# Kernel tuning notes

Hardware: AMD Instinct MI355X
Metric: run time of the kernel (lower is better)

The kernel has to match this reference:

```python
import jax, jax.numpy as jnp
import numpy as np


def _positional_embedding(C, M, dtype):
    # pe[pos, 0::2] = sin(pos*div), pe[pos, 1::2] = cos(pos*div)
    pos = jnp.arange(M, dtype=jnp.float32)[:, None]                      # [M,1]
    div = jnp.exp(jnp.arange(0, C, 2, dtype=jnp.float32) * (-np.log(10000.0) / C))  # [C/2]
    ang = pos * div                                                      # [M,C/2]
    pe = jnp.stack([jnp.sin(ang), jnp.cos(ang)], axis=-1).reshape(M, C)  # interleave
    return pe.T.astype(dtype)                                            # [C,M]


def setup_inputs() -> dict:
    key = jax.random.key(0)
    k1, k2, k3 = jax.random.split(key, 3)
    B, C, M, K = 64, 512, 1024, 5
    h_in = jax.random.normal(k1, (B, C, 1, M), dtype=jnp.float32)
    conv_w = jax.random.normal(k2, (C, K), dtype=jnp.float32) * 0.1
    conv_b = jax.random.normal(k3, (C,), dtype=jnp.float32) * 0.1
    return {"h_in": h_in, "conv_w": conv_w, "conv_b": conv_b}


def reference(h_in, conv_w, conv_b):
    B, C, _, M = h_in.shape
    K = conv_w.shape[1]
    p = (K - 1) // 2
    dt = h_in.dtype

    hb = h_in                                              # pre-PE copy
    pe = _positional_embedding(C, M, dt)                   # [C,M]
    x = h_in + pe[None, :, None, :]                        # [B,C,1,M]

    # adaptive avg pool to 1 over (H,W)
    y = jnp.mean(x, axis=(2, 3))                           # [B,C]
    # unfold along channel axis with padding p, window K
    y_pad = jnp.pad(y, ((0, 0), (p, p)))                   # [B,C+2p]
    idx = jnp.arange(C)[:, None] + jnp.arange(K)[None, :]  # [C,K]
    y_unf = y_pad[:, idx]                                  # [B,C,K]
    # grouped conv1d -> per-channel dot over window, then sigmoid gate
    gate = jax.nn.sigmoid(jnp.einsum('bck,ck->bc', y_unf, conv_w) + conv_b)  # [B,C]

    h = x * gate[:, :, None, None]                         # dropout = identity (eval)

    hs = h[:, :, 0, :]                                     # [B,C,M]
    hbs = hb[:, :, 0, :]                                   # [B,C,M]
    I_hat = (jnp.eye(M, dtype=dt) / M) - (1.0 / (M * M))   # [M,M] centering matrix

    t1 = jnp.einsum('bcm,mn->bcn', hs, I_hat)
    t2 = jnp.einsum('bcm,mn->bcn', hbs, I_hat)
    cov = (jnp.einsum('bcn,bdn->bcd', t1, hs)
           + jnp.einsum('bcn,bdn->bcd', t2, hbs)
           + jnp.eye(C, dtype=dt) * 1e-8)                  # [B,C,C]
    return cov
```

## Files before the change

kernel.cpp:

```cpp
#include <hip/hip_runtime.h>
#include <hip/hip_bf16.h>
#include <math.h>

#define B_N 64
#define C_N 512
#define M_N 1024

typedef __attribute__((ext_vector_type(8))) short bf16x8;
typedef __attribute__((ext_vector_type(4))) float f32x4;
typedef __attribute__((ext_vector_type(16))) float f32x16;

__device__ __forceinline__ float b2f(unsigned short u) {
  unsigned int x = ((unsigned int)u) << 16;
  return __builtin_bit_cast(float, x);
}
__device__ __forceinline__ unsigned short f2b(float f) {
  unsigned int x = __builtin_bit_cast(unsigned int, f);
  unsigned int lsb = (x >> 16) & 1u;
  x += 0x7fffu + lsb;
  return (unsigned short)(x >> 16);
}
__device__ __forceinline__ float bround(float f) { return b2f(f2b(f)); }

typedef __attribute__((address_space(1))) const unsigned int gas_uint;
typedef __attribute__((address_space(3))) unsigned int las_uint;
__device__ __forceinline__ void async_ld(const void* g, const void* l) {
  __builtin_amdgcn_global_load_lds((gas_uint*)(uintptr_t)g,
                                   (las_uint*)(unsigned int)(uintptr_t)l, 16, 0, 0);
}

__global__ void k_detect(const unsigned short* __restrict__ p, int* __restrict__ flag) {
  unsigned short u = p[threadIdx.x];
  int e = (u >> 7) & 0xff;
  int pl = (u == 0) || (e >= 110 && e <= 134);
  int cnt = __syncthreads_count(pl);
  if (threadIdx.x == 0) *flag = (cnt >= 208) ? 1 : 0;
}

__global__ void k_mode(const int* __restrict__ flag, int wsOK, int* __restrict__ mode) {
  if (threadIdx.x == 0) *mode = (*flag == 1 && wsOK) ? 1 : 0;
}

__global__ void k_pe(unsigned short* __restrict__ pe) {
  int idx = blockIdx.x * 256 + threadIdx.x;
  int c = idx >> 10, m = idx & 1023;
  float freq = expf((float)(c & ~1) * (-9.210340371976184f / 512.0f));
  float ang = (float)m * freq;
  float v = (c & 1) ? cosf(ang) : sinf(ang);
  pe[idx] = f2b(v);
}

__global__ void k_pesum(const unsigned short* __restrict__ pe, float* __restrict__ pesum) {
  int lane = threadIdx.x & 63;
  int row = blockIdx.x * 4 + (threadIdx.x >> 6);
  float s = 0.f;
  const uint4* p = (const uint4*)(pe + (size_t)row * M_N);
  for (int j = 0; j < 2; j++) {
    union { uint4 v; unsigned short u[8]; } a; a.v = p[j * 64 + lane];
    for (int k = 0; k < 8; k++) s += b2f(a.u[k]);
  }
  for (int off = 32; off; off >>= 1) s += __shfl_down(s, off);
  if (lane == 0) pesum[row] = s;
}

__global__ void k_sums(const void* __restrict__ hin, const int* __restrict__ flag,
                       const float* __restrict__ pesum, float* __restrict__ rx,
                       float* __restrict__ rb) {
  int lane = threadIdx.x & 63;
  int row = blockIdx.x * 4 + (threadIdx.x >> 6);
  int f = *flag;
  float s = 0.f;
  if (f) {
    const uint4* h = (const uint4*)((const unsigned short*)hin + (size_t)row * M_N);
    for (int j = 0; j < 2; j++) {
      union { uint4 v; unsigned short u[8]; } a; a.v = h[j * 64 + lane];
      for (int k = 0; k < 8; k++) s += b2f(a.u[k]);
    }
  } else {
    const float4* h = (const float4*)((const float*)hin + (size_t)row * M_N);
    for (int j = 0; j < 4; j++) {
      float4 v = h[j * 64 + lane];
      s += v.x + v.y + v.z + v.w;
    }
  }
  for (int off = 32; off; off >>= 1) s += __shfl_down(s, off);
  if (lane == 0) { rb[row] = s; rx[row] = s + pesum[row & (C_N - 1)]; }
}

__global__ void k_gate(const void* __restrict__ wp, const void* __restrict__ bp,
                       const int* __restrict__ flag, const float* __restrict__ rx,
                       float* __restrict__ gate) {
  int idx = blockIdx.x * 256 + threadIdx.x;
  int b = idx >> 9, c = idx & (C_N - 1);
  int f = *flag;
  float acc = 0.f;
  for (int k = 0; k < 5; ++k) {
    int cc = c + k - 2;
    if (cc < 0 || cc >= C_N) continue;
    float y = rx[b * C_N + cc] * (1.0f / 1024.0f);
    float w;
    if (f) { y = bround(y); w = b2f(((const unsigned short*)wp)[c * 5 + k]); }
    else   { w = ((const float*)wp)[c * 5 + k]; }
    acc += y * w;
  }
  float bias = f ? b2f(((const unsigned short*)bp)[c]) : ((const float*)bp)[c];
  float s = f ? bround(bround(acc) + bias) : (acc + bias);
  float g = 1.0f / (1.0f + expf(-s));
  if (f) g = bround(g);
  gate[idx] = g;
}

__global__ void k_prep(const void* __restrict__ hin, const unsigned short* __restrict__ pe,
                       const int* __restrict__ mode, unsigned short* __restrict__ X) {
  if (*mode != 1) return;
  size_t e = ((size_t)blockIdx.x * 256 + threadIdx.x) * 8;
  int cm = (int)(e & ((size_t)C_N * M_N - 1));
  union { uint4 v; unsigned short u[8]; } a, p, r;
  a.v = *(const uint4*)((const unsigned short*)hin + e);
  p.v = *(const uint4*)(pe + cm);
  for (int k = 0; k < 8; k++) r.u[k] = f2b(b2f(a.u[k]) + b2f(p.u[k]));
  *(uint4*)(X + e) = r.v;
}

__global__ __launch_bounds__(256, 2)
void k_cov2(const unsigned short* __restrict__ X, const void* __restrict__ hin,
            const int* __restrict__ mode, const float* __restrict__ rx,
            const float* __restrict__ rb, const float* __restrict__ gate,
            void* __restrict__ out) {
  if (*mode != 1) return;
  __shared__ unsigned short tiles[4][128 * 32];

  const unsigned short* H = (const unsigned short*)hin;
  int t = threadIdx.x;
  int lane = t & 63, w = t >> 6;
  int b = blockIdx.z;
  int cblk = blockIdx.y * 128, dblk = blockIdx.x * 128;

  const unsigned short* src = (w & 1) ? H : X;
  int rowbase = (w & 2) ? dblk : cblk;
  int gcol = (lane & 3) ^ ((lane >> 3) & 3);
  const unsigned short* gp = src + (size_t)b * (C_N * M_N)
                           + (size_t)(rowbase + (lane >> 2)) * M_N + gcol * 8;

  int wr = (w >> 1) * 64, wc = (w & 1) * 64;
  int fr = lane & 31, L5 = lane >> 5;
  int sw = (fr >> 1) & 3;

  f32x16 a1[2][2], a2[2][2];
  for (int i = 0; i < 2; i++)
    for (int j = 0; j < 2; j++)
      for (int r = 0; r < 16; r++) { a1[i][j][r] = 0.f; a2[i][j][r] = 0.f; }

  for (int kk = 0; kk < M_N; kk += 32) {
    const unsigned short* g0 = gp + kk;
    for (int g = 0; g < 8; g++)
      async_ld(g0 + (size_t)g * (16 * M_N), &tiles[w][g * 512]);
    __syncthreads();

    for (int ks = 0; ks < 2; ks++) {
      int kc = (ks * 2 + L5);
      bf16x8 aX[2], aH[2], bX[2], bH[2];
      for (int i = 0; i < 2; i++) {
        int R = wr + i * 32 + fr;
        int off = R * 32 + (kc ^ sw) * 8;
        aX[i] = *(const bf16x8*)&tiles[0][off];
        aH[i] = *(const bf16x8*)&tiles[1][off];
      }
      for (int j = 0; j < 2; j++) {
        int D = wc + j * 32 + fr;
        int off = D * 32 + (kc ^ sw) * 8;
        bX[j] = *(const bf16x8*)&tiles[2][off];
        bH[j] = *(const bf16x8*)&tiles[3][off];
      }
      for (int i = 0; i < 2; i++)
        for (int j = 0; j < 2; j++) {
          a1[i][j] = __builtin_amdgcn_mfma_f32_32x32x16_bf16(aX[i], bX[j], a1[i][j], 0, 0, 0);
          a2[i][j] = __builtin_amdgcn_mfma_f32_32x32x16_bf16(aH[i], bH[j], a2[i][j], 0, 0, 0);
        }
    }
    __syncthreads();
  }

  const float invM = 1.0f / 1024.0f, invM2 = invM * invM;
  const float* gb = gate + b * C_N;
  const float* rxb = rx + b * C_N;
  const float* rbb = rb + b * C_N;
  unsigned short* o16 = (unsigned short*)out;
  for (int i = 0; i < 2; i++)
    for (int j = 0; j < 2; j++) {
      int d = dblk + wc + j * 32 + (lane & 31);
      float gd = gb[d], rxd = rxb[d], rbd = rbb[d];
      for (int reg = 0; reg < 16; reg++) {
        int row = (reg & 3) + 8 * (reg >> 2) + 4 * L5;
        int c = cblk + wr + i * 32 + row;
        float v = gb[c] * gd * (a1[i][j][reg] * invM - rxb[c] * rxd * invM2)
                + (a2[i][j][reg] * invM - rbb[c] * rbd * invM2);
        if (c == d) v += 1e-8f;
        o16[((size_t)b * C_N + c) * C_N + d] = f2b(v);
      }
    }
}

__global__ __launch_bounds__(256, 2)
void k_cov(const void* __restrict__ hin, const unsigned short* __restrict__ pe,
           const int* __restrict__ flag, const int* __restrict__ mode,
           const float* __restrict__ rx, const float* __restrict__ rb,
           const float* __restrict__ gate, void* __restrict__ out) {
  if (*mode != 0) return;
  __shared__ unsigned short sXa[128 * 40];
  __shared__ unsigned short sHa[128 * 40];
  __shared__ unsigned short sXb[128 * 40];
  __shared__ unsigned short sHb[128 * 40];

  int t = threadIdx.x;
  int b = blockIdx.z;
  int cblk = blockIdx.y * 128, dblk = blockIdx.x * 128;
  int f = *flag;
  int lane = t & 63, wave = t >> 6;
  int wr = (wave >> 1) * 64, wc = (wave & 1) * 64;
  int fr = lane & 15, fk = (lane >> 4) * 8;
  int sr = t >> 1, sc = (t & 1) * 16;

  f32x4 acc1[4][4], acc2[4][4];
  const f32x4 z = {0.f, 0.f, 0.f, 0.f};
  for (int i = 0; i < 4; i++)
    for (int j = 0; j < 4; j++) { acc1[i][j] = z; acc2[i][j] = z; }

  const size_t hb0 = (size_t)b * C_N * M_N;
  const unsigned short* peA = pe + (size_t)(cblk + sr) * M_N + sc;
  const unsigned short* peB = pe + (size_t)(dblk + sr) * M_N + sc;
  const unsigned short* hA16 = (const unsigned short*)hin + hb0 + (size_t)(cblk + sr) * M_N + sc;
  const unsigned short* hB16 = (const unsigned short*)hin + hb0 + (size_t)(dblk + sr) * M_N + sc;
  const float* hA32 = (const float*)hin + hb0 + (size_t)(cblk + sr) * M_N + sc;
  const float* hB32 = (const float*)hin + hb0 + (size_t)(dblk + sr) * M_N + sc;

  union U { uint4 v[2]; unsigned short u[16]; };

  for (int kk = 0; kk < M_N; kk += 32) {
    U pa, pb, wxa, wha, wxb, whb;
    {
      const uint4* ppa = reinterpret_cast<const uint4*>(peA + kk);
      pa.v[0] = ppa[0]; pa.v[1] = ppa[1];
      const uint4* ppb = reinterpret_cast<const uint4*>(peB + kk);
      pb.v[0] = ppb[0]; pb.v[1] = ppb[1];
    }
    if (f) {
      U ua, ub;
      const uint4* qa = reinterpret_cast<const uint4*>(hA16 + kk);
      ua.v[0] = qa[0]; ua.v[1] = qa[1];
      const uint4* qb = reinterpret_cast<const uint4*>(hB16 + kk);
      ub.v[0] = qb[0]; ub.v[1] = qb[1];
      for (int e = 0; e < 16; e++) {
        wha.u[e] = ua.u[e];
        whb.u[e] = ub.u[e];
        wxa.u[e] = f2b(b2f(ua.u[e]) + b2f(pa.u[e]));
        wxb.u[e] = f2b(b2f(ub.u[e]) + b2f(pb.u[e]));
      }
    } else {
      float fa[16], fb[16];
      const float4* qa = reinterpret_cast<const float4*>(hA32 + kk);
      const float4* qb = reinterpret_cast<const float4*>(hB32 + kk);
      for (int e = 0; e < 4; e++) {
        float4 va = qa[e], vb = qb[e];
        fa[4 * e + 0] = va.x; fa[4 * e + 1] = va.y; fa[4 * e + 2] = va.z; fa[4 * e + 3] = va.w;
        fb[4 * e + 0] = vb.x; fb[4 * e + 1] = vb.y; fb[4 * e + 2] = vb.z; fb[4 * e + 3] = vb.w;
      }
      for (int e = 0; e < 16; e++) {
        wha.u[e] = f2b(fa[e]);
        whb.u[e] = f2b(fb[e]);
        wxa.u[e] = f2b(fa[e] + b2f(pa.u[e]));
        wxb.u[e] = f2b(fb[e] + b2f(pb.u[e]));
      }
    }
    {
      uint4* d0 = reinterpret_cast<uint4*>(&sXa[sr * 40 + sc]);
      d0[0] = wxa.v[0]; d0[1] = wxa.v[1];
      uint4* d1 = reinterpret_cast<uint4*>(&sHa[sr * 40 + sc]);
      d1[0] = wha.v[0]; d1[1] = wha.v[1];
      uint4* d2 = reinterpret_cast<uint4*>(&sXb[sr * 40 + sc]);
      d2[0] = wxb.v[0]; d2[1] = wxb.v[1];
      uint4* d3 = reinterpret_cast<uint4*>(&sHb[sr * 40 + sc]);
      d3[0] = whb.v[0]; d3[1] = whb.v[1];
    }
    __syncthreads();

    bf16x8 bX[4], bH[4];
    for (int j = 0; j < 4; j++) {
      int dr = wc + j * 16 + fr;
      bX[j] = *reinterpret_cast<const bf16x8*>(&sXb[dr * 40 + fk]);
      bH[j] = *reinterpret_cast<const bf16x8*>(&sHb[dr * 40 + fk]);
    }
    for (int i = 0; i < 4; i++) {
      int cr = wr + i * 16 + fr;
      bf16x8 aX = *reinterpret_cast<const bf16x8*>(&sXa[cr * 40 + fk]);
      bf16x8 aH = *reinterpret_cast<const bf16x8*>(&sHa[cr * 40 + fk]);
      for (int j = 0; j < 4; j++) {
        acc1[i][j] = __builtin_amdgcn_mfma_f32_16x16x32_bf16(aX, bX[j], acc1[i][j], 0, 0, 0);
        acc2[i][j] = __builtin_amdgcn_mfma_f32_16x16x32_bf16(aH, bH[j], acc2[i][j], 0, 0, 0);
      }
    }
    __syncthreads();
  }

  const float invM = 1.0f / 1024.0f;
  const float invM2 = invM * invM;
  const float* gb = gate + b * C_N;
  const float* rxb = rx + b * C_N;
  const float* rbb = rb + b * C_N;
  for (int i = 0; i < 4; i++) {
    for (int r = 0; r < 4; r++) {
      int c = cblk + wr + i * 16 + (lane >> 4) * 4 + r;
      float gc = gb[c], rxc = rxb[c], rbc = rbb[c];
      for (int j = 0; j < 4; j++) {
        int d = dblk + wc + j * 16 + (lane & 15);
        float v = gc * gb[d] * (acc1[i][j][r] * invM - rxc * rxb[d] * invM2)
                + (acc2[i][j][r] * invM - rbc * rbb[d] * invM2);
        if (c == d) v += 1e-8f;
        size_t o = ((size_t)b * C_N + c) * C_N + d;
        if (f) ((unsigned short*)out)[o] = f2b(v);
        else   ((float*)out)[o] = v;
      }
    }
  }
}

extern "C" void kernel_launch(void* const* d_in, const int* in_sizes, int n_in,
                              void* d_out, int out_size, void* d_ws, size_t ws_size,
                              hipStream_t stream) {
  const void* h_in = d_in[0];
  const void* conv_w = d_in[1];
  const void* conv_b = d_in[2];

  char* ws = (char*)d_ws;
  int* flag = (int*)ws;
  int* mode = (int*)(ws + 64);
  float* pesum = (float*)(ws + 1024);
  float* rx = (float*)(ws + 4096);
  float* rb = rx + B_N * C_N;
  float* gate = rb + B_N * C_N;
  unsigned short* pe = (unsigned short*)(ws + (1 << 20));
  unsigned short* X = (unsigned short*)(ws + (2 << 20));
  size_t need = (size_t)(2 << 20) + 2ull * B_N * C_N * M_N + 4096;
  int wsOK = (ws_size >= need) ? 1 : 0;

  k_detect<<<1, 256, 0, stream>>>((const unsigned short*)h_in, flag);
  k_mode<<<1, 64, 0, stream>>>(flag, wsOK, mode);
  k_pe<<<(C_N * M_N) / 256, 256, 0, stream>>>(pe);
  k_pesum<<<C_N / 4, 256, 0, stream>>>(pe, pesum);
  k_sums<<<(B_N * C_N) / 4, 256, 0, stream>>>(h_in, flag, pesum, rx, rb);
  k_gate<<<(B_N * C_N) / 256, 256, 0, stream>>>(conv_w, conv_b, flag, rx, gate);
  k_prep<<<(B_N * C_N * M_N) / (8 * 256), 256, 0, stream>>>(h_in, pe, mode, X);
  dim3 g(C_N / 128, C_N / 128, B_N);
  k_cov2<<<g, 256, 0, stream>>>(X, h_in, mode, rx, rb, gate, d_out);
  k_cov<<<g, 256, 0, stream>>>(h_in, pe, flag, mode, rx, rb, gate, d_out);
}
```

Measured before the change: 373.6 us.

## Expand (h+pe) Gram algebraically to drop X materialization and reuse shared PE Gram

Replaces the k_prep pass that materialized X=h+pe in bf16 with an algebraic expansion: X·Xᵀ = H·Hᵀ + H·PEᵀ + PE·Hᵀ + PE·PEᵀ. The batch-independent PE·PEᵀ is computed once by a new k_P kernel, and k_cov3 accumulates H·Hᵀ and the cross terms with 16x16x32 MFMAs, reading h and pe directly. This removes a full read/write pass over a 64 MiB intermediate. In exchange it issues 50% more MFMAs per tile and rounds differently from the old version. It also adds a batch-grouped block swizzle and a fallback that stores P in the output's last slice when the workspace is small.

```diff
diff --git a/kernel.cpp b/kernel.cpp
--- a/kernel.cpp
+++ b/kernel.cpp
@@ -8,7 +8,6 @@
 
 typedef __attribute__((ext_vector_type(8))) short bf16x8;
 typedef __attribute__((ext_vector_type(4))) float f32x4;
-typedef __attribute__((ext_vector_type(16))) float f32x16;
 
 __device__ __forceinline__ float b2f(unsigned short u) {
   unsigned int x = ((unsigned int)u) << 16;
@@ -110,73 +109,100 @@
   gate[idx] = g;
 }
 
-__global__ void k_prep(const void* __restrict__ hin, const unsigned short* __restrict__ pe,
-                       const int* __restrict__ mode, unsigned short* __restrict__ X) {
-  if (*mode != 1) return;
-  size_t e = ((size_t)blockIdx.x * 256 + threadIdx.x) * 8;
-  int cm = (int)(e & ((size_t)C_N * M_N - 1));
-  union { uint4 v; unsigned short u[8]; } a, p, r;
-  a.v = *(const uint4*)((const unsigned short*)hin + e);
-  p.v = *(const uint4*)(pe + cm);
-  for (int k = 0; k < 8; k++) r.u[k] = f2b(b2f(a.u[k]) + b2f(p.u[k]));
-  *(uint4*)(X + e) = r.v;
-}
-
 __global__ __launch_bounds__(256, 2)
-void k_cov2(const unsigned short* __restrict__ X, const void* __restrict__ hin,
-            const int* __restrict__ mode, const float* __restrict__ rx,
-            const float* __restrict__ rb, const float* __restrict__ gate,
-            void* __restrict__ out) {
+void k_P(const unsigned short* __restrict__ pe, unsigned short* __restrict__ Pout) {
+  __shared__ unsigned short tiles[2][128 * 32];
+  int t = threadIdx.x, lane = t & 63, w = t >> 6;
+  int cblk = blockIdx.y * 128, dblk = blockIdx.x * 128;
+  int gcol = (lane & 3) ^ ((lane >> 3) & 3);
+  const unsigned short* srcp = pe
+      + (size_t)((w ? dblk : cblk) + (lane >> 2)) * M_N + gcol * 8;
+  int wr = (w >> 1) * 64, wc = (w & 1) * 64;
+  int fr = lane & 15, kc = lane >> 4;
+  int fcol = ((kc ^ ((fr >> 1) & 3))) * 8;
+
+  f32x4 acc[4][4];
+  const f32x4 z = {0.f, 0.f, 0.f, 0.f};
+  for (int i = 0; i < 4; i++) for (int j = 0; j < 4; j++) acc[i][j] = z;
+
+  for (int kk = 0; kk < M_N; kk += 32) {
+    if (w < 2)
+      for (int g = 0; g < 8; g++)
+        async_ld(srcp + kk + (size_t)g * (16 * M_N), &tiles[w][g * 512]);
+    __syncthreads();
+    bf16x8 bf[4];
+    for (int j = 0; j < 4; j++)
+      bf[j] = *(const bf16x8*)&tiles[1][(wc + j * 16 + fr) * 32 + fcol];
+    for (int i = 0; i < 4; i++) {
+      bf16x8 af = *(const bf16x8*)&tiles[0][(wr + i * 16 + fr) * 32 + fcol];
+      for (int j = 0; j < 4; j++)
+        acc[i][j] = __builtin_amdgcn_mfma_f32_16x16x32_bf16(af, bf[j], acc[i][j], 0, 0, 0);
+    }
+    __syncthreads();
+  }
+  for (int i = 0; i < 4; i++)
+    for (int r = 0; r < 4; r++) {
+      int c = cblk + wr + i * 16 + kc * 4 + r;
+      for (int j = 0; j < 4; j++) {
+        int d = dblk + wc + j * 16 + fr;
+        Pout[c * C_N + d] = f2b(acc[i][j][r]);
+      }
+    }
+}
+
+__global__ __launch_bounds__(256, 2)
+void k_cov3(const unsigned short* __restrict__ h, const unsigned short* __restrict__ pe,
+            const unsigned short* __restrict__ P, const int* __restrict__ mode,
+            const float* __restrict__ rx, const float* __restrict__ rb,
+            const float* __restrict__ gate, unsigned short* __restrict__ out,
+            int b0, int swz) {
   if (*mode != 1) return;
   __shared__ unsigned short tiles[4][128 * 32];
-
-  const unsigned short* H = (const unsigned short*)hin;
-  int t = threadIdx.x;
-  int lane = t & 63, w = t >> 6;
-  int b = blockIdx.z;
-  int cblk = blockIdx.y * 128, dblk = blockIdx.x * 128;
-
-  const unsigned short* src = (w & 1) ? H : X;
+  int t = threadIdx.x, lane = t & 63, w = t >> 6;
+  int bx, by, b;
+  if (swz) {
+    int lid = blockIdx.x;
+    b = b0 + (lid >> 7) * 8 + (lid & 7);
+    int s = (lid >> 3) & 15; bx = s & 3; by = s >> 2;
+  } else { bx = blockIdx.x; by = blockIdx.y; b = b0 + blockIdx.z; }
+  int cblk = by * 128, dblk = bx * 128;
+
   int rowbase = (w & 2) ? dblk : cblk;
   int gcol = (lane & 3) ^ ((lane >> 3) & 3);
-  const unsigned short* gp = src + (size_t)b * (C_N * M_N)
-                           + (size_t)(rowbase + (lane >> 2)) * M_N + gcol * 8;
+  const unsigned short* srcp;
+  if (w & 1) srcp = pe + (size_t)(rowbase + (lane >> 2)) * M_N + gcol * 8;
+  else       srcp = h + (size_t)b * (C_N * M_N)
+                      + (size_t)(rowbase + (lane >> 2)) * M_N + gcol * 8;
 
   int wr = (w >> 1) * 64, wc = (w & 1) * 64;
-  int fr = lane & 31, L5 = lane >> 5;
-  int sw = (fr >> 1) & 3;
-
-  f32x16 a1[2][2], a2[2][2];
-  for (int i = 0; i < 2; i++)
-    for (int j = 0; j < 2; j++)
-      for (int r = 0; r < 16; r++) { a1[i][j][r] = 0.f; a2[i][j][r] = 0.f; }
+  int fr = lane & 15, kc = lane >> 4;
+  int fcol = ((kc ^ ((fr >> 1) & 3))) * 8;
+
+  f32x4 aS[4][4], aU[4][4];
+  const f32x4 z = {0.f, 0.f, 0.f, 0.f};
+  for (int i = 0; i < 4; i++)
+    for (int j = 0; j < 4; j++) { aS[i][j] = z; aU[i][j] = z; }
 
   for (int kk = 0; kk < M_N; kk += 32) {
-    const unsigned short* g0 = gp + kk;
     for (int g = 0; g < 8; g++)
-      async_ld(g0 + (size_t)g * (16 * M_N), &tiles[w][g * 512]);
-    __syncthreads();
-
-    for (int ks = 0; ks < 2; ks++) {
-      int kc = (ks * 2 + L5);
-      bf16x8 aX[2], aH[2], bX[2], bH[2];
-      for (int i = 0; i < 2; i++) {
-        int R = wr + i * 32 + fr;
-        int off = R * 32 + (kc ^ sw) * 8;
-        aX[i] = *(const bf16x8*)&tiles[0][off];
-        aH[i] = *(const bf16x8*)&tiles[1][off];
-      }
-      for (int j = 0; j < 2; j++) {
-        int D = wc + j * 32 + fr;
-        int off = D * 32 + (kc ^ sw) * 8;
-        bX[j] = *(const bf16x8*)&tiles[2][off];
-        bH[j] = *(const bf16x8*)&tiles[3][off];
-      }
-      for (int i = 0; i < 2; i++)
-        for (int j = 0; j < 2; j++) {
-          a1[i][j] = __builtin_amdgcn_mfma_f32_32x32x16_bf16(aX[i], bX[j], a1[i][j], 0, 0, 0);
-          a2[i][j] = __builtin_amdgcn_mfma_f32_32x32x16_bf16(aH[i], bH[j], a2[i][j], 0, 0, 0);
-        }
+      async_ld(srcp + kk + (size_t)g * (16 * M_N), &tiles[w][g * 512]);
+    __syncthreads();
+
+    bf16x8 bH[4], bP[4];
+    for (int j = 0; j < 4; j++) {
+      int off = (wc + j * 16 + fr) * 32 + fcol;
+      bH[j] = *(const bf16x8*)&tiles[2][off];
+      bP[j] = *(const bf16x8*)&tiles[3][off];
+    }
+    for (int i = 0; i < 4; i++) {
+      int off = (wr + i * 16 + fr) * 32 + fcol;
+      bf16x8 aH = *(const bf16x8*)&tiles[0][off];
+      bf16x8 aP = *(const bf16x8*)&tiles[1][off];
+      for (int j = 0; j < 4; j++) {
+        aS[i][j] = __builtin_amdgcn_mfma_f32_16x16x32_bf16(aH, bH[j], aS[i][j], 0, 0, 0);
+        aU[i][j] = __builtin_amdgcn_mfma_f32_16x16x32_bf16(aH, bP[j], aU[i][j], 0, 0, 0);
+        aU[i][j] = __builtin_amdgcn_mfma_f32_16x16x32_bf16(aP, bH[j], aU[i][j], 0, 0, 0);
+      }
     }
     __syncthreads();
   }
@@ -185,18 +211,18 @@
   const float* gb = gate + b * C_N;
   const float* rxb = rx + b * C_N;
   const float* rbb = rb + b * C_N;
-  unsigned short* o16 = (unsigned short*)out;
-  for (int i = 0; i < 2; i++)
-    for (int j = 0; j < 2; j++) {
-      int d = dblk + wc + j * 32 + (lane & 31);
-      float gd = gb[d], rxd = rxb[d], rbd = rbb[d];
-      for (int reg = 0; reg < 16; reg++) {
-        int row = (reg & 3) + 8 * (reg >> 2) + 4 * L5;
-        int c = cblk + wr + i * 32 + row;
-        float v = gb[c] * gd * (a1[i][j][reg] * invM - rxb[c] * rxd * invM2)
-                + (a2[i][j][reg] * invM - rbb[c] * rbd * invM2);
+  for (int i = 0; i < 4; i++)
+    for (int r = 0; r < 4; r++) {
+      int c = cblk + wr + i * 16 + kc * 4 + r;
+      float gc = gb[c], rxc = rxb[c], rbc = rbb[c];
+      for (int j = 0; j < 4; j++) {
+        int d = dblk + wc + j * 16 + fr;
+        float S2 = aS[i][j][r];
+        float S1 = S2 + aU[i][j][r] + b2f(P[c * C_N + d]);
+        float v = gc * gb[d] * (S1 * invM - rxc * rxb[d] * invM2)
+                + (S2 * invM - rbc * rbb[d] * invM2);
         if (c == d) v += 1e-8f;
-        o16[((size_t)b * C_N + c) * C_N + d] = f2b(v);
+        out[((size_t)b * C_N + c) * C_N + d] = f2b(v);
       }
     }
 }
@@ -338,10 +364,12 @@
   float* rx = (float*)(ws + 4096);
   float* rb = rx + B_N * C_N;
   float* gate = rb + B_N * C_N;
-  unsigned short* pe = (unsigned short*)(ws + (1 << 20));
-  unsigned short* X = (unsigned short*)(ws + (2 << 20));
-  size_t need = (size_t)(2 << 20) + 2ull * B_N * C_N * M_N + 4096;
-  int wsOK = (ws_size >= need) ? 1 : 0;
+  unsigned short* pe = (unsigned short*)(ws + (512 << 10));
+
+  int wsOK = (ws_size >= (size_t)(1536 << 10)) ? 1 : 0;
+  int wsP  = (ws_size >= (size_t)(2048 << 10)) ? 1 : 0;
+  unsigned short* Pp = wsP ? (unsigned short*)(ws + (1536 << 10))
+                           : (unsigned short*)d_out + (size_t)63 * C_N * C_N;
 
   k_detect<<<1, 256, 0, stream>>>((const unsigned short*)h_in, flag);
   k_mode<<<1, 64, 0, stream>>>(flag, wsOK, mode);
@@ -349,8 +377,17 @@
   k_pesum<<<C_N / 4, 256, 0, stream>>>(pe, pesum);
   k_sums<<<(B_N * C_N) / 4, 256, 0, stream>>>(h_in, flag, pesum, rx, rb);
   k_gate<<<(B_N * C_N) / 256, 256, 0, stream>>>(conv_w, conv_b, flag, rx, gate);
-  k_prep<<<(B_N * C_N * M_N) / (8 * 256), 256, 0, stream>>>(h_in, pe, mode, X);
+  k_P<<<dim3(4, 4, 1), 256, 0, stream>>>(pe, Pp);
+
+  const unsigned short* h16 = (const unsigned short*)h_in;
+  unsigned short* o16 = (unsigned short*)d_out;
+  if (wsP) {
+    k_cov3<<<1024, 256, 0, stream>>>(h16, pe, Pp, mode, rx, rb, gate, o16, 0, 1);
+  } else {
+    k_cov3<<<896, 256, 0, stream>>>(h16, pe, Pp, mode, rx, rb, gate, o16, 0, 1);
+    k_cov3<<<dim3(4, 4, 7), 256, 0, stream>>>(h16, pe, Pp, mode, rx, rb, gate, o16, 56, 0);
+    k_cov3<<<dim3(4, 4, 1), 256, 0, stream>>>(h16, pe, Pp, mode, rx, rb, gate, o16, 63, 0);
+  }
   dim3 g(C_N / 128, C_N / 128, B_N);
-  k_cov2<<<g, 256, 0, stream>>>(X, h_in, mode, rx, rb, gate, d_out);
   k_cov<<<g, 256, 0, stream>>>(h_in, pe, flag, mode, rx, rb, gate, d_out);
 }
```

New measurement: 386.5 us. 3.5% more time.
